# Performance work log

Measured on AMD Instinct MI355X. Metric: run time of the kernel, lower is better.

## Reference

```python
import jax, jax.numpy as jnp
import numpy as np

N_U, N_P, E, E_LAB = 100000, 50000, 2000000, 500000
D_U, D_P, H = 64, 128, 64


def _seg_mean(feat, idx, n):
    # scatter-mean: sum per destination / clamp(count, 1)
    s = jax.ops.segment_sum(feat, idx, num_segments=n)
    c = jax.ops.segment_sum(jnp.ones((idx.shape[0],), feat.dtype), idx, num_segments=n)
    return s / jnp.maximum(c, 1.0)[:, None]


def setup_inputs() -> dict:
    key = jax.random.key(0)
    ks = jax.random.split(key, 16)
    inp = {
        'x_user': jax.random.normal(ks[0], (N_U, D_U), jnp.float32),
        'x_product': jax.random.normal(ks[1], (N_P, D_P), jnp.float32),
        'W1_buys_l': jax.random.normal(ks[2], (D_U, H), jnp.float32) * 0.05,
        'b1_buys': jnp.zeros((H,), jnp.float32),
        'W1_buys_r': jax.random.normal(ks[3], (D_P, H), jnp.float32) * 0.05,
        'W1_rev_l': jax.random.normal(ks[4], (D_P, H), jnp.float32) * 0.05,
        'b1_rev': jnp.zeros((H,), jnp.float32),
        'W1_rev_r': jax.random.normal(ks[5], (D_U, H), jnp.float32) * 0.05,
        'W2_buys_l': jax.random.normal(ks[6], (H, H), jnp.float32) * 0.05,
        'b2_buys': jnp.zeros((H,), jnp.float32),
        'W2_buys_r': jax.random.normal(ks[7], (H, H), jnp.float32) * 0.05,
        'W2_rev_l': jax.random.normal(ks[8], (H, H), jnp.float32) * 0.05,
        'b2_rev': jnp.zeros((H,), jnp.float32),
        'W2_rev_r': jax.random.normal(ks[9], (H, H), jnp.float32) * 0.05,
        'edge_src': jax.random.randint(ks[10], (E,), 0, N_U, jnp.int32),
        'edge_dst': jax.random.randint(ks[11], (E,), 0, N_P, jnp.int32),
        'lab_u': jax.random.randint(ks[12], (E_LAB,), 0, N_U, jnp.int32),
        'lab_p': jax.random.randint(ks[13], (E_LAB,), 0, N_P, jnp.int32),
    }
    return inp


def reference(x_user, x_product, W1_buys_l, b1_buys, W1_buys_r, W1_rev_l, b1_rev, W1_rev_r,
              W2_buys_l, b2_buys, W2_buys_r, W2_rev_l, b2_rev, W2_rev_r,
              edge_src, edge_dst, lab_u, lab_p):
    # SAGEConv (mean aggr): out_dst = mean_agg(x_src) @ W_l + b + x_dst @ W_r
    def sage(x_src, x_dst, src, dst, n_dst, Wl, b, Wr):
        agg = _seg_mean(x_src[src], dst, n_dst)
        return agg @ Wl + b + x_dst @ Wr

    n_u, n_p = x_user.shape[0], x_product.shape[0]
    # layer 1 (per edge type, hetero) + relu
    h_p = jax.nn.relu(sage(x_user, x_product, edge_src, edge_dst, n_p, W1_buys_l, b1_buys, W1_buys_r))
    h_u = jax.nn.relu(sage(x_product, x_user, edge_dst, edge_src, n_u, W1_rev_l, b1_rev, W1_rev_r))
    # layer 2
    h_p2 = sage(h_u, h_p, edge_src, edge_dst, n_p, W2_buys_l, b2_buys, W2_buys_r)
    h_u2 = sage(h_p, h_u, edge_dst, edge_src, n_u, W2_rev_l, b2_rev, W2_rev_r)
    # classifier: per-label-edge dot product
    return jnp.sum(h_u2[lab_u] * h_p2[lab_p], axis=-1)
```

## Files before the change

kernel.cpp:

```cpp
#include <hip/hip_runtime.h>


using u16 = unsigned short;
using u32 = unsigned int;

__device__ __forceinline__ u16 bf16r(float f) {
    u32 b = __float_as_uint(f);
    b += 0x7fffu + ((b >> 16) & 1u);
    return (u16)(b >> 16);
}
__device__ __forceinline__ float2 bfup(u32 u) {
    return make_float2(__uint_as_float(u << 16), __uint_as_float(u & 0xffff0000u));
}

#define BSH 8
#define MAXB 512
#define CHUNK 4096
#define RPT 16

#define FMA_ROW(ACC, O, W4) \
    ACC[0] += (O) * (W4).x; ACC[1] += (O) * (W4).y; \
    ACC[2] += (O) * (W4).z; ACC[3] += (O) * (W4).w;

__global__ __launch_bounds__(256) void k_partCast(
    const int* __restrict__ keysP, const int* __restrict__ payP,
    int* __restrict__ curPp, uint2* __restrict__ pairsP, int NBP, int SLP,
    const int* __restrict__ keysU, const int* __restrict__ payU,
    int* __restrict__ curUp, uint2* __restrict__ pairsU, int NBU, int SLU,
    int E, int pblocks,
    const int* __restrict__ keysL,
    int* __restrict__ curLp, uint2* __restrict__ pairsL, int NBL, int SLL,
    int EL, int lblocks,
    const float* __restrict__ xc, u16* __restrict__ yc, int n8,
    int ctStart, int g128,
    const float* __restrict__ xp, const float* __restrict__ Wrl,
    const float* __restrict__ Wbr, u16* __restrict__ bfB,
    float* __restrict__ h_p, float* __restrict__ sinkF,
    u16* __restrict__ sinkB, int NPc) {
    __shared__ __align__(16) char smem[49664];
    int tid = threadIdx.x;
    int bix = blockIdx.x;
    if (bix >= ctStart) {
        float* Ws = (float*)smem;
        float* op = (float*)(smem + 32768);
        int cbix = bix - ctStart;
        const float* W; float* h; u16* hbf;
        int bid;
        if (cbix < g128) { W = Wrl; h = sinkF; hbf = bfB;   bid = cbix; }
        else             { W = Wbr; h = h_p;   hbf = sinkB; bid = cbix - g128; }
        for (int i = tid; i < 128 * 16; i += 256)
            ((float4*)Ws)[i] = ((const float4*)W)[i];
        const int c4 = (tid & 15) * 4;
        const int rb = (tid >> 4) * 2;
        const int ntiles = (NPc + 31) / 32;
        for (int tile = bid; tile < ntiles; tile += g128) {
            const int row0 = tile * 32;
            __syncthreads();
            for (int i = tid; i < 32 * 32; i += 256) {
                int r = i >> 5, k4 = (i & 31) * 4;
                int row = row0 + r;
                float4 v = make_float4(0.f, 0.f, 0.f, 0.f);
                if (row < NPc) v = *(const float4*)(xp + (size_t)row * 128 + k4);
                *(float4*)(op + r * 132 + k4) = v;
            }
            __syncthreads();
            float acc[2][4];
#pragma unroll
            for (int i = 0; i < 2; ++i) {
                acc[i][0] = 0.f; acc[i][1] = 0.f; acc[i][2] = 0.f; acc[i][3] = 0.f;
            }
            for (int kk = 0; kk < 128; kk += 4) {
                float4 w0 = *(const float4*)(Ws + (kk + 0) * 64 + c4);
                float4 w1 = *(const float4*)(Ws + (kk + 1) * 64 + c4);
                float4 w2 = *(const float4*)(Ws + (kk + 2) * 64 + c4);
                float4 w3 = *(const float4*)(Ws + (kk + 3) * 64 + c4);
#pragma unroll
                for (int i = 0; i < 2; ++i) {
                    float4 o = *(const float4*)(op + (rb + i) * 132 + kk);
                    FMA_ROW(acc[i], o.x, w0);
                    FMA_ROW(acc[i], o.y, w1);
                    FMA_ROW(acc[i], o.z, w2);
                    FMA_ROW(acc[i], o.w, w3);
                }
            }
#pragma unroll
            for (int i = 0; i < 2; ++i) {
                int row = row0 + rb + i;
                if (row >= NPc) continue;
                float v0 = acc[i][0], v1 = acc[i][1], v2 = acc[i][2], v3 = acc[i][3];
                *(float4*)(h + (size_t)row * 64 + c4) = make_float4(v0, v1, v2, v3);
                uint2 o;
                o.x = (u32)bf16r(v0) | ((u32)bf16r(v1) << 16);
                o.y = (u32)bf16r(v2) | ((u32)bf16r(v3) << 16);
                *(uint2*)(hbf + (size_t)row * 64 + c4) = o;
            }
        }
        return;
    }
    if (bix >= 2 * pblocks + lblocks) {
        int i = (bix - 2 * pblocks - lblocks) * 256 + tid;
        if (i < n8) {
            const float4* x4 = (const float4*)xc;
            float4 a = x4[i * 2], b = x4[i * 2 + 1];
            uint4 o;
            o.x = (u32)bf16r(a.x) | ((u32)bf16r(a.y) << 16);
            o.y = (u32)bf16r(a.z) | ((u32)bf16r(a.w) << 16);
            o.z = (u32)bf16r(b.x) | ((u32)bf16r(b.y) << 16);
            o.w = (u32)bf16r(b.z) | ((u32)bf16r(b.w) << 16);
            ((uint4*)yc)[i] = o;
        }
        return;
    }
    int* hist   = (int*)smem;
    int* sA     = (int*)(smem + 2048);
    int* sB     = (int*)(smem + 4096);
    int* bx     = (int*)(smem + 6144);
    int* gbase  = (int*)(smem + 8192);
    uint2* prs  = (uint2*)(smem + 10240);
    const int* keys; const int* pay; int* cursor; uint2* pairs;
    int NB, SL, cb, nE;
    if (bix < pblocks) {
        keys = keysP; pay = payP; cursor = curPp; pairs = pairsP; NB = NBP; SL = SLP;
        cb = bix; nE = E;
    } else if (bix < 2 * pblocks) {
        keys = keysU; pay = payU; cursor = curUp; pairs = pairsU; NB = NBU; SL = SLU;
        cb = bix - pblocks; nE = E;
    } else {
        keys = keysL; pay = nullptr; cursor = curLp; pairs = pairsL; NB = NBL; SL = SLL;
        cb = bix - 2 * pblocks; nE = EL;
    }
    int i0 = cb * CHUNK;
    int count = min(CHUNK, nE - i0);
    for (int i = tid; i < MAXB; i += 256) hist[i] = 0;
    __syncthreads();
    int keyr[RPT], payr[RPT], rankr[RPT];
#pragma unroll
    for (int r = 0; r < RPT; ++r) {
        int idx = r * 256 + tid;
        if (idx < count) {
            int k = keys[i0 + idx];
            keyr[r] = k;
            payr[r] = pay ? pay[i0 + idx] : (i0 + idx);
            rankr[r] = atomicAdd(&hist[k >> BSH], 1);
        } else keyr[r] = -1;
    }
    __syncthreads();
    sA[tid] = hist[tid]; sA[tid + 256] = hist[tid + 256];
    __syncthreads();
    int* src = sA; int* dst = sB;
    for (int off = 1; off < MAXB; off <<= 1) {
        dst[tid] = src[tid] + ((tid >= off) ? src[tid - off] : 0);
        int i2 = tid + 256;
        dst[i2] = src[i2] + ((i2 >= off) ? src[i2 - off] : 0);
        __syncthreads();
        int* t = src; src = dst; dst = t;
    }
    bx[tid] = src[tid] - hist[tid];
    bx[tid + 256] = src[tid + 256] - hist[tid + 256];
    __syncthreads();
    for (int b = tid; b < NB; b += 256) {
        int c = hist[b];
        gbase[b] = c ? (b * SL + atomicAdd(&cursor[b], c)) : 0;
    }
#pragma unroll
    for (int r = 0; r < RPT; ++r) {
        if (keyr[r] >= 0)
            prs[bx[keyr[r] >> BSH] + rankr[r]] = make_uint2((u32)keyr[r], (u32)payr[r]);
    }
    __syncthreads();
    for (int j = tid; j < count; j += 256) {
        uint2 pr = prs[j];
        int b = pr.x >> BSH;
        pairs[gbase[b] + (j - bx[b])] = pr;
    }
}

__global__ __launch_bounds__(256) void k_bucketFill(
    const uint2* __restrict__ pairsP, const int* __restrict__ cntP, int NBP, int SLP,
    int* __restrict__ nbr_p, int* __restrict__ deg_p, int* __restrict__ ptr_p, int NP,
    const uint2* __restrict__ pairsU, const int* __restrict__ cntU, int NBU, int SLU,
    int* __restrict__ nbr_u, int* __restrict__ deg_u, int* __restrict__ ptr_u, int NU) {
    const uint2* pairs; const int* cntA; int* nbr; int* deg; int* ptr;
    int N, SL, bucket;
    if ((int)blockIdx.x < NBP) {
        pairs = pairsP; cntA = cntP; nbr = nbr_p; deg = deg_p; ptr = ptr_p; N = NP;
        SL = SLP; bucket = blockIdx.x;
    } else {
        pairs = pairsU; cntA = cntU; nbr = nbr_u; deg = deg_u; ptr = ptr_u; N = NU;
        SL = SLU; bucket = blockIdx.x - NBP;
    }
    int tid = threadIdx.x;
    int base = bucket * SL;
    int cnt = cntA[bucket];
    __shared__ int h[256];
    __shared__ int s[256];
    __shared__ int cur[256];
    h[tid] = 0;
    __syncthreads();
    for (int j = tid; j < cnt; j += 256) atomicAdd(&h[pairs[base + j].x & 255], 1);
    __syncthreads();
    int d = h[tid];
    s[tid] = d;
    __syncthreads();
    for (int off = 1; off < 256; off <<= 1) {
        int v = (tid >= off) ? s[tid - off] : 0;
        __syncthreads();
        s[tid] += v;
        __syncthreads();
    }
    int excl = s[tid] - d;
    int node = bucket * 256 + tid;
    if (node < N) { deg[node] = d; ptr[node] = base + excl; }
    cur[tid] = excl;
    __syncthreads();
    for (int j = tid; j < cnt; j += 256) {
        uint2 pr = pairs[base + j];
        int pos = atomicAdd(&cur[pr.x & 255], 1);
        nbr[base + pos] = (int)(pr.y << 7);
    }
}

#define ACC8(A01,A23,A45,A67,V) \
    A01 += bfup((V).x); A23 += bfup((V).y); A45 += bfup((V).z); A67 += bfup((V).w);

__global__ __launch_bounds__(256) void k_gather2(
    const u16* __restrict__ yA, const int* __restrict__ nbrA, const int* __restrict__ stpA,
    const int* __restrict__ degA, float* __restrict__ aggA, int NA,
    const u16* __restrict__ yB, const int* __restrict__ nbrB, const int* __restrict__ stpB,
    const int* __restrict__ degB, float* __restrict__ aggB, int NB) {
    int w = (blockIdx.x * 256 + threadIdx.x) >> 6;
    int lane = threadIdx.x & 63;
    if (w >= NA + NB) return;
    const u16* y; const int* nbr; const int* stp; const int* deg; float* agg; int n;
    if (w < NA) { y = yA; nbr = nbrA; stp = stpA; deg = degA; agg = aggA; n = w; }
    else        { y = yB; nbr = nbrB; stp = stpB; deg = degB; agg = aggB; n = w - NA; }
    const int q = lane >> 3, t = lane & 7;
    const int d = deg[n];
    const int st = stp[n];
    const char* yb = (const char*)y + t * 16;
    float2 a01 = make_float2(0.f, 0.f), a23 = make_float2(0.f, 0.f);
    float2 a45 = make_float2(0.f, 0.f), a67 = make_float2(0.f, 0.f);
    for (int j = 0; j < d; j += 64) {
        const int cnt = min(d - j, 64);
        int offv = 0;
        if (lane < cnt) offv = nbr[st + j + lane];
#define GLD(R) \
        int g##R = __shfl(offv, R * 8 + q, 64); \
        uint4 v##R = make_uint4(0u, 0u, 0u, 0u); \
        if (R * 8 + q < cnt) v##R = *(const uint4*)(yb + g##R);
        GLD(0) GLD(1) GLD(2) GLD(3) GLD(4) GLD(5) GLD(6) GLD(7)
#undef GLD
#define ACCR(R) if (R * 8 < cnt) { ACC8(a01,a23,a45,a67,v##R) }
        ACCR(0) ACCR(1) ACCR(2) ACCR(3) ACCR(4) ACCR(5) ACCR(6) ACCR(7)
#undef ACCR
    }
#pragma unroll
    for (int m = 8; m < 64; m <<= 1) {
        a01.x += __shfl_xor(a01.x, m, 64); a01.y += __shfl_xor(a01.y, m, 64);
        a23.x += __shfl_xor(a23.x, m, 64); a23.y += __shfl_xor(a23.y, m, 64);
        a45.x += __shfl_xor(a45.x, m, 64); a45.y += __shfl_xor(a45.y, m, 64);
        a67.x += __shfl_xor(a67.x, m, 64); a67.y += __shfl_xor(a67.y, m, 64);
    }
    if (q == 0) {
        float dinv = 1.0f / (float)max(d, 1);
        float* dstp = agg + n * 64 + t * 8;
        *(float4*)dstp       = make_float4(a01.x * dinv, a01.y * dinv, a23.x * dinv, a23.y * dinv);
        *(float4*)(dstp + 4) = make_float4(a45.x * dinv, a45.y * dinv, a67.x * dinv, a67.y * dinv);
    }
}

template <int K, bool PRE, bool BIAS, bool RELU, bool EMIT>
__global__ __launch_bounds__(256) void k_ctilePairX(
    const float* __restrict__ pre0, const float* __restrict__ bias0,
    const float* __restrict__ x0, const float* __restrict__ W0,
    float* __restrict__ h0, u16* __restrict__ hbf0, int N0, int g0,
    const float* __restrict__ pre1, const float* __restrict__ bias1,
    const float* __restrict__ x1, const float* __restrict__ W1,
    float* __restrict__ h1, u16* __restrict__ hbf1, int N1) {
    constexpr int ROWS = (K == 64) ? 64 : 32;
    constexpr int RR = ROWS / 16;
    constexpr int STRIDE = K + 4;
    constexpr int KF4 = K / 4;
    __shared__ float Ws[K * 64];
    __shared__ float op[ROWS * STRIDE];
    const float* pre; const float* bias; const float* x; const float* W;
    float* h; u16* hbf;
    int N, bid, gsz;
    if ((int)blockIdx.x < g0) {
        pre = pre0; bias = bias0; x = x0; W = W0; h = h0; hbf = hbf0; N = N0;
        bid = blockIdx.x; gsz = g0;
    } else {
        pre = pre1; bias = bias1; x = x1; W = W1; h = h1; hbf = hbf1; N = N1;
        bid = blockIdx.x - g0; gsz = gridDim.x - g0;
    }
    const int tid = threadIdx.x;
    for (int i = tid; i < K * 16; i += 256)
        ((float4*)Ws)[i] = ((const float4*)W)[i];
    const int c4 = (tid & 15) * 4;
    const int rb = (tid >> 4) * RR;
    float bx_ = 0.f, by_ = 0.f, bz_ = 0.f, bw_ = 0.f;
    if (BIAS) {
        float4 b4 = *(const float4*)(bias + c4);
        bx_ = b4.x; by_ = b4.y; bz_ = b4.z; bw_ = b4.w;
    }
    const int ntiles = (N + ROWS - 1) / ROWS;
    for (int tile = bid; tile < ntiles; tile += gsz) {
        const int row0 = tile * ROWS;
        __syncthreads();
        for (int i = tid; i < ROWS * KF4; i += 256) {
            int r = i / KF4, k4 = (i % KF4) * 4;
            int row = row0 + r;
            float4 v = make_float4(0.f, 0.f, 0.f, 0.f);
            if (row < N) v = *(const float4*)(x + (size_t)row * K + k4);
            *(float4*)(op + r * STRIDE + k4) = v;
        }
        __syncthreads();
        float acc[RR][4];
#pragma unroll
        for (int i = 0; i < RR; ++i) {
            float px = 0.f, py = 0.f, pz = 0.f, pw = 0.f;
            if (PRE) {
                int row = row0 + rb + i;
                if (row < N) {
                    float4 p = *(const float4*)(pre + row * 64 + c4);
                    px = p.x; py = p.y; pz = p.z; pw = p.w;
                }
            }
            acc[i][0] = bx_ + px; acc[i][1] = by_ + py;
            acc[i][2] = bz_ + pz; acc[i][3] = bw_ + pw;
        }
        for (int kk = 0; kk < K; kk += 4) {
            float4 w0 = *(const float4*)(Ws + (kk + 0) * 64 + c4);
            float4 w1 = *(const float4*)(Ws + (kk + 1) * 64 + c4);
            float4 w2 = *(const float4*)(Ws + (kk + 2) * 64 + c4);
            float4 w3 = *(const float4*)(Ws + (kk + 3) * 64 + c4);
#pragma unroll
            for (int i = 0; i < RR; ++i) {
                float4 o = *(const float4*)(op + (rb + i) * STRIDE + kk);
                FMA_ROW(acc[i], o.x, w0);
                FMA_ROW(acc[i], o.y, w1);
                FMA_ROW(acc[i], o.z, w2);
                FMA_ROW(acc[i], o.w, w3);
            }
        }
#pragma unroll
        for (int i = 0; i < RR; ++i) {
            int row = row0 + rb + i;
            if (row >= N) continue;
            float v0 = acc[i][0], v1 = acc[i][1], v2 = acc[i][2], v3 = acc[i][3];
            if (RELU) {
                v0 = fmaxf(v0, 0.f); v1 = fmaxf(v1, 0.f);
                v2 = fmaxf(v2, 0.f); v3 = fmaxf(v3, 0.f);
            }
            *(float4*)(h + row * 64 + c4) = make_float4(v0, v1, v2, v3);
            if (EMIT) {
                uint2 o;
                o.x = (u32)bf16r(v0) | ((u32)bf16r(v1) << 16);
                o.y = (u32)bf16r(v2) | ((u32)bf16r(v3) << 16);
                *(uint2*)(hbf + row * 64 + c4) = o;
            }
        }
    }
}

template <bool BIAS>
__global__ __launch_bounds__(256) void k_ctilePairCat(
    const float* __restrict__ bias0, const float* __restrict__ xa0,
    const float* __restrict__ xb0, const float* __restrict__ Wa0,
    const float* __restrict__ Wb0, float* __restrict__ h0, int N0, int g0,
    const float* __restrict__ bias1, const float* __restrict__ xa1,
    const float* __restrict__ xb1, const float* __restrict__ Wa1,
    const float* __restrict__ Wb1, float* __restrict__ h1, int N1) {
    constexpr int ROWS = 32, RR = 2, STRIDE = 132, KF4 = 32;
    __shared__ float Ws[128 * 64];
    __shared__ float op[ROWS * STRIDE];
    const float* bias; const float* xa; const float* xb;
    const float* Wa; const float* Wb; float* h;
    int N, bid, gsz;
    if ((int)blockIdx.x < g0) {
        bias = bias0; xa = xa0; xb = xb0; Wa = Wa0; Wb = Wb0; h = h0; N = N0;
        bid = blockIdx.x; gsz = g0;
    } else {
        bias = bias1; xa = xa1; xb = xb1; Wa = Wa1; Wb = Wb1; h = h1; N = N1;
        bid = blockIdx.x - g0; gsz = gridDim.x - g0;
    }
    const int tid = threadIdx.x;
    for (int i = tid; i < 64 * 16; i += 256) {
        ((float4*)Ws)[i]           = ((const float4*)Wa)[i];
        ((float4*)Ws)[64 * 16 + i] = ((const float4*)Wb)[i];
    }
    const int c4 = (tid & 15) * 4;
    const int rb = (tid >> 4) * RR;
    float bx_ = 0.f, by_ = 0.f, bz_ = 0.f, bw_ = 0.f;
    if (BIAS) {
        float4 b4 = *(const float4*)(bias + c4);
        bx_ = b4.x; by_ = b4.y; bz_ = b4.z; bw_ = b4.w;
    }
    const int ntiles = (N + ROWS - 1) / ROWS;
    for (int tile = bid; tile < ntiles; tile += gsz) {
        const int row0 = tile * ROWS;
        __syncthreads();
        for (int i = tid; i < ROWS * KF4; i += 256) {
            int r = i >> 5, k4 = (i & 31) * 4;
            int row = row0 + r;
            float4 v = make_float4(0.f, 0.f, 0.f, 0.f);
            if (row < N)
                v = (k4 < 64) ? *(const float4*)(xa + (size_t)row * 64 + k4)
                              : *(const float4*)(xb + (size_t)row * 64 + (k4 - 64));
            *(float4*)(op + r * STRIDE + k4) = v;
        }
        __syncthreads();
        float acc[RR][4];
#pragma unroll
        for (int i = 0; i < RR; ++i) {
            acc[i][0] = bx_; acc[i][1] = by_; acc[i][2] = bz_; acc[i][3] = bw_;
        }
        for (int kk = 0; kk < 128; kk += 4) {
            float4 w0 = *(const float4*)(Ws + (kk + 0) * 64 + c4);
            float4 w1 = *(const float4*)(Ws + (kk + 1) * 64 + c4);
            float4 w2 = *(const float4*)(Ws + (kk + 2) * 64 + c4);
            float4 w3 = *(const float4*)(Ws + (kk + 3) * 64 + c4);
#pragma unroll
            for (int i = 0; i < RR; ++i) {
                float4 o = *(const float4*)(op + (rb + i) * STRIDE + kk);
                FMA_ROW(acc[i], o.x, w0);
                FMA_ROW(acc[i], o.y, w1);
                FMA_ROW(acc[i], o.z, w2);
                FMA_ROW(acc[i], o.w, w3);
            }
        }
#pragma unroll
        for (int i = 0; i < RR; ++i) {
            int row = row0 + rb + i;
            if (row >= N) continue;
            *(float4*)(h + row * 64 + c4) =
                make_float4(acc[i][0], acc[i][1], acc[i][2], acc[i][3]);
        }
    }
}

__global__ __launch_bounds__(256) void k_classifyS(const float* __restrict__ hu,
                                                   const float* __restrict__ hp,
                                                   const int* __restrict__ lu,
                                                   const uint2* __restrict__ pairsL,
                                                   const int* __restrict__ cntL,
                                                   int lsh,
                                                   float* __restrict__ out, int nslots) {
    int w = (blockIdx.x * 256 + threadIdx.x) >> 6;
    int lane = threadIdx.x & 63;
    int q = lane >> 4, t = lane & 15;
    int slot = w * 4 + q;
    float v = 0.f;
    int e = 0;
    bool ok = false;
    if (slot < nslots) {
        int bucket = slot >> lsh;
        int within = slot & ((1 << lsh) - 1);
        if (within < cntL[bucket]) {
            uint2 pr = pairsL[slot];
            int p = (int)pr.x;
            e = (int)pr.y;
            int u = lu[e];
            float4 a = *(const float4*)(hu + (size_t)u * 64 + t * 4);
            float4 b = *(const float4*)(hp + (size_t)p * 64 + t * 4);
            v = a.x * b.x + a.y * b.y + a.z * b.z + a.w * b.w;
            ok = true;
        }
    }
#pragma unroll
    for (int m = 1; m < 16; m <<= 1) v += __shfl_xor(v, m, 64);
    if (t == 0 && ok) out[e] = v;
}

extern "C" void kernel_launch(void* const* d_in, const int* in_sizes, int n_in,
                              void* d_out, int out_size, void* d_ws, size_t ws_size,
                              hipStream_t stream) {
    const float* x_user    = (const float*)d_in[0];
    const float* x_product = (const float*)d_in[1];
    const float* W1bl = (const float*)d_in[2];
    const float* b1b  = (const float*)d_in[3];
    const float* W1br = (const float*)d_in[4];
    const float* W1rl = (const float*)d_in[5];
    const float* b1r  = (const float*)d_in[6];
    const float* W1rr = (const float*)d_in[7];
    const float* W2bl = (const float*)d_in[8];
    const float* b2b  = (const float*)d_in[9];
    const float* W2br = (const float*)d_in[10];
    const float* W2rl = (const float*)d_in[11];
    const float* b2r  = (const float*)d_in[12];
    const float* W2rr = (const float*)d_in[13];
    const int* esrc = (const int*)d_in[14];
    const int* edst = (const int*)d_in[15];
    const int* lu   = (const int*)d_in[16];
    const int* lp   = (const int*)d_in[17];

    const int NU = in_sizes[0] / 64;
    const int NP = in_sizes[1] / 128;
    const int E  = in_sizes[14];
    const int EL = in_sizes[16];
    const int NBP = (NP + 255) >> BSH;
    const int NBU = (NU + 255) >> BSH;
    const int NBL = NBP;

    const int SLP = E / NBP + E / (NBP * 8) + 1024;
    const int SLU = E / NBU + E / (NBU * 8) + 1024;
    int lneed = EL / NBL + EL / (NBL * 4) + 512;
    int lsh = 1;
    while ((1 << lsh) < lneed) ++lsh;
    const int SLL = 1 << lsh;

    char* ws = (char*)d_ws;
    size_t off = 0;
    auto alloc = [&](size_t bytes) -> void* {
        void* p = ws + off;
        off += (bytes + 255) & ~(size_t)255;
        return p;
    };
    int*   deg_u  = (int*)alloc((size_t)NU * 4);
    int*   deg_p  = (int*)alloc((size_t)NP * 4);
    int*   ptr_u  = (int*)alloc((size_t)NU * 4);
    int*   ptr_p  = (int*)alloc((size_t)NP * 4);
    int*   curP   = (int*)alloc((size_t)MAXB * 4);
    int*   curU   = (int*)alloc((size_t)MAXB * 4);
    int*   curL   = (int*)alloc((size_t)MAXB * 4);
    int*   nbr_u  = (int*)alloc((size_t)NBU * SLU * 4);
    int*   nbr_p  = (int*)alloc((size_t)NBP * SLP * 4);
    uint2* pairsL = (uint2*)alloc((size_t)NBL * SLL * 8);
    size_t aggBytes = (size_t)(NP + NU) * 64 * 4;
    size_t pairBytes = ((size_t)NBP * SLP + (size_t)NBU * SLU) * 8;
    char* uni = (char*)alloc(aggBytes > pairBytes ? aggBytes : pairBytes);
    float* aggP   = (float*)uni;
    float* aggU   = (float*)(uni + (size_t)NP * 64 * 4);
    uint2* pairsP = (uint2*)uni;
    uint2* pairsU = (uint2*)(uni + (size_t)NBP * SLP * 8);
    u16*   bfA    = (u16*)alloc((size_t)NU * 64 * 2);
    u16*   bfB    = (u16*)alloc((size_t)NP * 64 * 2);
    float* h_p    = (float*)alloc((size_t)NP * 64 * 4);
    float* h_u    = (float*)alloc((size_t)NU * 64 * 4);
    float* sinkF  = h_u;
    u16*   sinkB  = (u16*)((char*)h_u + (size_t)NP * 64 * 4);

    const int tP32 = (NP + 31) / 32;
    const int tU32 = (NU + 31) / 32;
    const int tP64 = (NP + 63) / 64, tU64 = (NU + 63) / 64;
    auto cap = [](int t, int c) { return t < c ? t : c; };

    hipMemsetAsync(curP, 0, (size_t)MAXB * 3 * 4, stream);
    const int n8 = NU * 64 / 8;
    const int castBlocks = (n8 + 255) / 256;
    const int pblocks = (E + CHUNK - 1) / CHUNK;
    const int lblocks = (EL + CHUNK - 1) / CHUNK;
    const int g128 = cap(tP32, 768);
    const int ctStart = 2 * pblocks + lblocks + castBlocks;
    k_partCast<<<ctStart + 2 * g128, 256, 0, stream>>>(
        edst, esrc, curP, pairsP, NBP, SLP,
        esrc, edst, curU, pairsU, NBU, SLU, E, pblocks,
        lp, curL, pairsL, NBL, SLL, EL, lblocks,
        x_user, bfA, n8,
        ctStart, g128,
        x_product, W1rl, W1br, bfB, h_p, sinkF, sinkB, NP);
    k_bucketFill<<<NBP + NBU, 256, 0, stream>>>(
        pairsP, curP, NBP, SLP, nbr_p, deg_p, ptr_p, NP,
        pairsU, curU, NBU, SLU, nbr_u, deg_u, ptr_u, NU);

    k_gather2<<<(NP + NU + 3) / 4, 256, 0, stream>>>(bfA, nbr_p, ptr_p, deg_p, aggP, NP,
                                                     bfB, nbr_u, ptr_u, deg_u, aggU, NU);
    {
        const int gP = cap(tP64, 512), gU = cap(tU64, 1024);
        k_ctilePairX<64, true, true, true, true><<<gP + gU, 256, 0, stream>>>(
            h_p, b1b, aggP, W1bl, h_p, bfB, NP, gP,
            aggU, b1r, x_user, W1rr, h_u, bfA, NU);
    }

    k_gather2<<<(NP + NU + 3) / 4, 256, 0, stream>>>(bfA, nbr_p, ptr_p, deg_p, aggP, NP,
                                                     bfB, nbr_u, ptr_u, deg_u, aggU, NU);
    {
        const int gP = cap(tP32, 512), gU = cap(tU32, 1024);
        k_ctilePairCat<true><<<gP + gU, 256, 0, stream>>>(
            b2b, aggP, h_p, W2bl, W2br, h_p, NP, gP,
            b2r, aggU, h_u, W2rl, W2rr, h_u, NU);
    }

    const int nslots = NBL << lsh;
    k_classifyS<<<((nslots + 3) / 4 + 3) / 4, 256, 0, stream>>>(
        h_u, h_p, lu, pairsL, curL, lsh, (float*)d_out, nslots);
}
```

Measured before the change: 481.2 us.

## Replace bucket-sort CSR build with direct atomic scatter into fixed-slot adjacency

Drops the two-pass partition plus bucket-fill CSR construction. Each edge is now scattered straight into a fixed-capacity per-node slot array using a global atomicAdd on a per-node counter, and the gather reads from node*SL with degree min(cnt, SL). The label-edge sort is also removed, so the classifier reads lu/lp directly. This cuts one kernel launch and the sort traffic, but relies on node degrees staying under 2*avg+48 or 2*avg+24. Edges past that capacity are silently dropped while the count still includes them, so the mean is wrong for high-degree nodes.

```diff
diff --git a/kernel.cpp b/kernel.cpp
--- a/kernel.cpp
+++ b/kernel.cpp
@@ -13,41 +13,29 @@
     return make_float2(__uint_as_float(u << 16), __uint_as_float(u & 0xffff0000u));
 }
 
-#define BSH 8
-#define MAXB 512
-#define CHUNK 4096
-#define RPT 16
-
 #define FMA_ROW(ACC, O, W4) \
     ACC[0] += (O) * (W4).x; ACC[1] += (O) * (W4).y; \
     ACC[2] += (O) * (W4).z; ACC[3] += (O) * (W4).w;
 
-__global__ __launch_bounds__(256) void k_partCast(
-    const int* __restrict__ keysP, const int* __restrict__ payP,
-    int* __restrict__ curPp, uint2* __restrict__ pairsP, int NBP, int SLP,
-    const int* __restrict__ keysU, const int* __restrict__ payU,
-    int* __restrict__ curUp, uint2* __restrict__ pairsU, int NBU, int SLU,
-    int E, int pblocks,
-    const int* __restrict__ keysL,
-    int* __restrict__ curLp, uint2* __restrict__ pairsL, int NBL, int SLL,
-    int EL, int lblocks,
-    const float* __restrict__ xc, u16* __restrict__ yc, int n8,
-    int ctStart, int g128,
+__global__ __launch_bounds__(256) void k_buildAll(
+    const int* __restrict__ esrc, const int* __restrict__ edst, int E,
+    int* __restrict__ cntP, int* __restrict__ nbrP, int SLPn,
+    int* __restrict__ cntU, int* __restrict__ nbrU, int SLUn,
+    int g128, int sStart, int cStart, int NPc,
     const float* __restrict__ xp, const float* __restrict__ Wrl,
     const float* __restrict__ Wbr, u16* __restrict__ bfB,
-    float* __restrict__ h_p, float* __restrict__ sinkF,
-    u16* __restrict__ sinkB, int NPc) {
+    float* __restrict__ h_p, float* __restrict__ sinkF, u16* __restrict__ sinkB,
+    const float* __restrict__ xc, u16* __restrict__ yc, int n8) {
     __shared__ __align__(16) char smem[49664];
     int tid = threadIdx.x;
     int bix = blockIdx.x;
-    if (bix >= ctStart) {
+    if (bix < 2 * g128) {
         float* Ws = (float*)smem;
         float* op = (float*)(smem + 32768);
-        int cbix = bix - ctStart;
         const float* W; float* h; u16* hbf;
         int bid;
-        if (cbix < g128) { W = Wrl; h = sinkF; hbf = bfB;   bid = cbix; }
-        else             { W = Wbr; h = h_p;   hbf = sinkB; bid = cbix - g128; }
+        if (bix < g128) { W = Wrl; h = sinkF; hbf = bfB;   bid = bix; }
+        else            { W = Wbr; h = h_p;   hbf = sinkB; bid = bix - g128; }
         for (int i = tid; i < 128 * 16; i += 256)
             ((float4*)Ws)[i] = ((const float4*)W)[i];
         const int c4 = (tid & 15) * 4;
@@ -97,126 +85,36 @@
         }
         return;
     }
-    if (bix >= 2 * pblocks + lblocks) {
-        int i = (bix - 2 * pblocks - lblocks) * 256 + tid;
-        if (i < n8) {
-            const float4* x4 = (const float4*)xc;
-            float4 a = x4[i * 2], b = x4[i * 2 + 1];
-            uint4 o;
-            o.x = (u32)bf16r(a.x) | ((u32)bf16r(a.y) << 16);
-            o.y = (u32)bf16r(a.z) | ((u32)bf16r(a.w) << 16);
-            o.z = (u32)bf16r(b.x) | ((u32)bf16r(b.y) << 16);
-            o.w = (u32)bf16r(b.z) | ((u32)bf16r(b.w) << 16);
-            ((uint4*)yc)[i] = o;
-        }
+    if (bix < cStart) {
+        int i = (bix - sStart) * 256 + tid;
+        int E4 = E >> 2;
+#define SCAT(U, P) { \
+        int pp = atomicAdd(&cntP[P], 1); \
+        if (pp < SLPn) nbrP[(size_t)(P) * SLPn + pp] = (U) << 7; \
+        int pu = atomicAdd(&cntU[U], 1); \
+        if (pu < SLUn) nbrU[(size_t)(U) * SLUn + pu] = (P) << 7; }
+        if (i < E4) {
+            int4 s = ((const int4*)esrc)[i];
+            int4 d = ((const int4*)edst)[i];
+            SCAT(s.x, d.x) SCAT(s.y, d.y) SCAT(s.z, d.z) SCAT(s.w, d.w)
+        }
+        if (bix == sStart && tid < (E & 3)) {
+            int e = E4 * 4 + tid;
+            SCAT(esrc[e], edst[e])
+        }
+#undef SCAT
         return;
     }
-    int* hist   = (int*)smem;
-    int* sA     = (int*)(smem + 2048);
-    int* sB     = (int*)(smem + 4096);
-    int* bx     = (int*)(smem + 6144);
-    int* gbase  = (int*)(smem + 8192);
-    uint2* prs  = (uint2*)(smem + 10240);
-    const int* keys; const int* pay; int* cursor; uint2* pairs;
-    int NB, SL, cb, nE;
-    if (bix < pblocks) {
-        keys = keysP; pay = payP; cursor = curPp; pairs = pairsP; NB = NBP; SL = SLP;
-        cb = bix; nE = E;
-    } else if (bix < 2 * pblocks) {
-        keys = keysU; pay = payU; cursor = curUp; pairs = pairsU; NB = NBU; SL = SLU;
-        cb = bix - pblocks; nE = E;
-    } else {
-        keys = keysL; pay = nullptr; cursor = curLp; pairs = pairsL; NB = NBL; SL = SLL;
-        cb = bix - 2 * pblocks; nE = EL;
-    }
-    int i0 = cb * CHUNK;
-    int count = min(CHUNK, nE - i0);
-    for (int i = tid; i < MAXB; i += 256) hist[i] = 0;
-    __syncthreads();
-    int keyr[RPT], payr[RPT], rankr[RPT];
-#pragma unroll
-    for (int r = 0; r < RPT; ++r) {
-        int idx = r * 256 + tid;
-        if (idx < count) {
-            int k = keys[i0 + idx];
-            keyr[r] = k;
-            payr[r] = pay ? pay[i0 + idx] : (i0 + idx);
-            rankr[r] = atomicAdd(&hist[k >> BSH], 1);
-        } else keyr[r] = -1;
-    }
-    __syncthreads();
-    sA[tid] = hist[tid]; sA[tid + 256] = hist[tid + 256];
-    __syncthreads();
-    int* src = sA; int* dst = sB;
-    for (int off = 1; off < MAXB; off <<= 1) {
-        dst[tid] = src[tid] + ((tid >= off) ? src[tid - off] : 0);
-        int i2 = tid + 256;
-        dst[i2] = src[i2] + ((i2 >= off) ? src[i2 - off] : 0);
-        __syncthreads();
-        int* t = src; src = dst; dst = t;
-    }
-    bx[tid] = src[tid] - hist[tid];
-    bx[tid + 256] = src[tid + 256] - hist[tid + 256];
-    __syncthreads();
-    for (int b = tid; b < NB; b += 256) {
-        int c = hist[b];
-        gbase[b] = c ? (b * SL + atomicAdd(&cursor[b], c)) : 0;
-    }
-#pragma unroll
-    for (int r = 0; r < RPT; ++r) {
-        if (keyr[r] >= 0)
-            prs[bx[keyr[r] >> BSH] + rankr[r]] = make_uint2((u32)keyr[r], (u32)payr[r]);
-    }
-    __syncthreads();
-    for (int j = tid; j < count; j += 256) {
-        uint2 pr = prs[j];
-        int b = pr.x >> BSH;
-        pairs[gbase[b] + (j - bx[b])] = pr;
-    }
-}
-
-__global__ __launch_bounds__(256) void k_bucketFill(
-    const uint2* __restrict__ pairsP, const int* __restrict__ cntP, int NBP, int SLP,
-    int* __restrict__ nbr_p, int* __restrict__ deg_p, int* __restrict__ ptr_p, int NP,
-    const uint2* __restrict__ pairsU, const int* __restrict__ cntU, int NBU, int SLU,
-    int* __restrict__ nbr_u, int* __restrict__ deg_u, int* __restrict__ ptr_u, int NU) {
-    const uint2* pairs; const int* cntA; int* nbr; int* deg; int* ptr;
-    int N, SL, bucket;
-    if ((int)blockIdx.x < NBP) {
-        pairs = pairsP; cntA = cntP; nbr = nbr_p; deg = deg_p; ptr = ptr_p; N = NP;
-        SL = SLP; bucket = blockIdx.x;
-    } else {
-        pairs = pairsU; cntA = cntU; nbr = nbr_u; deg = deg_u; ptr = ptr_u; N = NU;
-        SL = SLU; bucket = blockIdx.x - NBP;
-    }
-    int tid = threadIdx.x;
-    int base = bucket * SL;
-    int cnt = cntA[bucket];
-    __shared__ int h[256];
-    __shared__ int s[256];
-    __shared__ int cur[256];
-    h[tid] = 0;
-    __syncthreads();
-    for (int j = tid; j < cnt; j += 256) atomicAdd(&h[pairs[base + j].x & 255], 1);
-    __syncthreads();
-    int d = h[tid];
-    s[tid] = d;
-    __syncthreads();
-    for (int off = 1; off < 256; off <<= 1) {
-        int v = (tid >= off) ? s[tid - off] : 0;
-        __syncthreads();
-        s[tid] += v;
-        __syncthreads();
-    }
-    int excl = s[tid] - d;
-    int node = bucket * 256 + tid;
-    if (node < N) { deg[node] = d; ptr[node] = base + excl; }
-    cur[tid] = excl;
-    __syncthreads();
-    for (int j = tid; j < cnt; j += 256) {
-        uint2 pr = pairs[base + j];
-        int pos = atomicAdd(&cur[pr.x & 255], 1);
-        nbr[base + pos] = (int)(pr.y << 7);
+    int i = (bix - cStart) * 256 + tid;
+    if (i < n8) {
+        const float4* x4 = (const float4*)xc;
+        float4 a = x4[i * 2], b = x4[i * 2 + 1];
+        uint4 o;
+        o.x = (u32)bf16r(a.x) | ((u32)bf16r(a.y) << 16);
+        o.y = (u32)bf16r(a.z) | ((u32)bf16r(a.w) << 16);
+        o.z = (u32)bf16r(b.x) | ((u32)bf16r(b.y) << 16);
+        o.w = (u32)bf16r(b.z) | ((u32)bf16r(b.w) << 16);
+        ((uint4*)yc)[i] = o;
     }
 }
 
@@ -224,19 +122,19 @@
     A01 += bfup((V).x); A23 += bfup((V).y); A45 += bfup((V).z); A67 += bfup((V).w);
 
 __global__ __launch_bounds__(256) void k_gather2(
-    const u16* __restrict__ yA, const int* __restrict__ nbrA, const int* __restrict__ stpA,
-    const int* __restrict__ degA, float* __restrict__ aggA, int NA,
-    const u16* __restrict__ yB, const int* __restrict__ nbrB, const int* __restrict__ stpB,
-    const int* __restrict__ degB, float* __restrict__ aggB, int NB) {
+    const u16* __restrict__ yA, const int* __restrict__ nbrA,
+    const int* __restrict__ cntA, int SLA, float* __restrict__ aggA, int NA,
+    const u16* __restrict__ yB, const int* __restrict__ nbrB,
+    const int* __restrict__ cntB, int SLB, float* __restrict__ aggB, int NB) {
     int w = (blockIdx.x * 256 + threadIdx.x) >> 6;
     int lane = threadIdx.x & 63;
     if (w >= NA + NB) return;
-    const u16* y; const int* nbr; const int* stp; const int* deg; float* agg; int n;
-    if (w < NA) { y = yA; nbr = nbrA; stp = stpA; deg = degA; agg = aggA; n = w; }
-    else        { y = yB; nbr = nbrB; stp = stpB; deg = degB; agg = aggB; n = w - NA; }
+    const u16* y; const int* nbr; const int* cntp; float* agg; int n, SL;
+    if (w < NA) { y = yA; nbr = nbrA; cntp = cntA; agg = aggA; n = w; SL = SLA; }
+    else        { y = yB; nbr = nbrB; cntp = cntB; agg = aggB; n = w - NA; SL = SLB; }
     const int q = lane >> 3, t = lane & 7;
-    const int d = deg[n];
-    const int st = stp[n];
+    const int d = min(cntp[n], SL);
+    const int st = n * SL;
     const char* yb = (const char*)y + t * 16;
     float2 a01 = make_float2(0.f, 0.f), a23 = make_float2(0.f, 0.f);
     float2 a45 = make_float2(0.f, 0.f), a67 = make_float2(0.f, 0.f);
@@ -439,37 +337,25 @@
     }
 }
 
-__global__ __launch_bounds__(256) void k_classifyS(const float* __restrict__ hu,
+__global__ __launch_bounds__(256) void k_classify4(const float* __restrict__ hu,
                                                    const float* __restrict__ hp,
                                                    const int* __restrict__ lu,
-                                                   const uint2* __restrict__ pairsL,
-                                                   const int* __restrict__ cntL,
-                                                   int lsh,
-                                                   float* __restrict__ out, int nslots) {
+                                                   const int* __restrict__ lp,
+                                                   float* __restrict__ out, int EL) {
     int w = (blockIdx.x * 256 + threadIdx.x) >> 6;
     int lane = threadIdx.x & 63;
     int q = lane >> 4, t = lane & 15;
-    int slot = w * 4 + q;
+    int e = w * 4 + q;
     float v = 0.f;
-    int e = 0;
-    bool ok = false;
-    if (slot < nslots) {
-        int bucket = slot >> lsh;
-        int within = slot & ((1 << lsh) - 1);
-        if (within < cntL[bucket]) {
-            uint2 pr = pairsL[slot];
-            int p = (int)pr.x;
-            e = (int)pr.y;
-            int u = lu[e];
-            float4 a = *(const float4*)(hu + (size_t)u * 64 + t * 4);
-            float4 b = *(const float4*)(hp + (size_t)p * 64 + t * 4);
-            v = a.x * b.x + a.y * b.y + a.z * b.z + a.w * b.w;
-            ok = true;
-        }
+    if (e < EL) {
+        int u = lu[e], p = lp[e];
+        float4 a = *(const float4*)(hu + (size_t)u * 64 + t * 4);
+        float4 b = *(const float4*)(hp + (size_t)p * 64 + t * 4);
+        v = a.x * b.x + a.y * b.y + a.z * b.z + a.w * b.w;
     }
 #pragma unroll
     for (int m = 1; m < 16; m <<= 1) v += __shfl_xor(v, m, 64);
-    if (t == 0 && ok) out[e] = v;
+    if (t == 0 && e < EL) out[e] = v;
 }
 
 extern "C" void kernel_launch(void* const* d_in, const int* in_sizes, int n_in,
@@ -498,16 +384,9 @@
     const int NP = in_sizes[1] / 128;
     const int E  = in_sizes[14];
     const int EL = in_sizes[16];
-    const int NBP = (NP + 255) >> BSH;
-    const int NBU = (NU + 255) >> BSH;
-    const int NBL = NBP;
-
-    const int SLP = E / NBP + E / (NBP * 8) + 1024;
-    const int SLU = E / NBU + E / (NBU * 8) + 1024;
-    int lneed = EL / NBL + EL / (NBL * 4) + 512;
-    int lsh = 1;
-    while ((1 << lsh) < lneed) ++lsh;
-    const int SLL = 1 << lsh;
+
+    const int SLPn = 2 * (E / NP) + 48;
+    const int SLUn = 2 * (E / NU) + 24;
 
     char* ws = (char*)d_ws;
     size_t off = 0;
@@ -516,23 +395,12 @@
         off += (bytes + 255) & ~(size_t)255;
         return p;
     };
-    int*   deg_u  = (int*)alloc((size_t)NU * 4);
-    int*   deg_p  = (int*)alloc((size_t)NP * 4);
-    int*   ptr_u  = (int*)alloc((size_t)NU * 4);
-    int*   ptr_p  = (int*)alloc((size_t)NP * 4);
-    int*   curP   = (int*)alloc((size_t)MAXB * 4);
-    int*   curU   = (int*)alloc((size_t)MAXB * 4);
-    int*   curL   = (int*)alloc((size_t)MAXB * 4);
-    int*   nbr_u  = (int*)alloc((size_t)NBU * SLU * 4);
-    int*   nbr_p  = (int*)alloc((size_t)NBP * SLP * 4);
-    uint2* pairsL = (uint2*)alloc((size_t)NBL * SLL * 8);
-    size_t aggBytes = (size_t)(NP + NU) * 64 * 4;
-    size_t pairBytes = ((size_t)NBP * SLP + (size_t)NBU * SLU) * 8;
-    char* uni = (char*)alloc(aggBytes > pairBytes ? aggBytes : pairBytes);
-    float* aggP   = (float*)uni;
-    float* aggU   = (float*)(uni + (size_t)NP * 64 * 4);
-    uint2* pairsP = (uint2*)uni;
-    uint2* pairsU = (uint2*)(uni + (size_t)NBP * SLP * 8);
+    int*   cntP   = (int*)alloc(((size_t)NP + NU) * 4);
+    int*   cntU   = cntP + NP;
+    int*   nbr_p  = (int*)alloc((size_t)NP * SLPn * 4);
+    int*   nbr_u  = (int*)alloc((size_t)NU * SLUn * 4);
+    float* aggP   = (float*)alloc((size_t)NP * 64 * 4);
+    float* aggU   = (float*)alloc((size_t)NU * 64 * 4);
     u16*   bfA    = (u16*)alloc((size_t)NU * 64 * 2);
     u16*   bfB    = (u16*)alloc((size_t)NP * 64 * 2);
     float* h_p    = (float*)alloc((size_t)NP * 64 * 4);
@@ -545,26 +413,24 @@
     const int tP64 = (NP + 63) / 64, tU64 = (NU + 63) / 64;
     auto cap = [](int t, int c) { return t < c ? t : c; };
 
-    hipMemsetAsync(curP, 0, (size_t)MAXB * 3 * 4, stream);
+    hipMemsetAsync(cntP, 0, ((size_t)NP + NU) * 4, stream);
     const int n8 = NU * 64 / 8;
     const int castBlocks = (n8 + 255) / 256;
-    const int pblocks = (E + CHUNK - 1) / CHUNK;
-    const int lblocks = (EL + CHUNK - 1) / CHUNK;
+    const int sblocks = ((E >> 2) + 255) / 256;
     const int g128 = cap(tP32, 768);
-    const int ctStart = 2 * pblocks + lblocks + castBlocks;
-    k_partCast<<<ctStart + 2 * g128, 256, 0, stream>>>(
-        edst, esrc, curP, pairsP, NBP, SLP,
-        esrc, edst, curU, pairsU, NBU, SLU, E, pblocks,
-        lp, curL, pairsL, NBL, SLL, EL, lblocks,
-        x_user, bfA, n8,
-        ctStart, g128,
-        x_product, W1rl, W1br, bfB, h_p, sinkF, sinkB, NP);
-    k_bucketFill<<<NBP + NBU, 256, 0, stream>>>(
-        pairsP, curP, NBP, SLP, nbr_p, deg_p, ptr_p, NP,
-        pairsU, curU, NBU, SLU, nbr_u, deg_u, ptr_u, NU);
-
-    k_gather2<<<(NP + NU + 3) / 4, 256, 0, stream>>>(bfA, nbr_p, ptr_p, deg_p, aggP, NP,
-                                                     bfB, nbr_u, ptr_u, deg_u, aggU, NU);
+    const int sStart = 2 * g128;
+    const int cStart = sStart + sblocks;
+    k_buildAll<<<cStart + castBlocks, 256, 0, stream>>>(
+        esrc, edst, E,
+        cntP, nbr_p, SLPn,
+        cntU, nbr_u, SLUn,
+        g128, sStart, cStart, NP,
+        x_product, W1rl, W1br, bfB, h_p, sinkF, sinkB,
+        x_user, bfA, n8);
+
+    k_gather2<<<(NP + NU + 3) / 4, 256, 0, stream>>>(
+        bfA, nbr_p, cntP, SLPn, aggP, NP,
+        bfB, nbr_u, cntU, SLUn, aggU, NU);
     {
         const int gP = cap(tP64, 512), gU = cap(tU64, 1024);
         k_ctilePairX<64, true, true, true, true><<<gP + gU, 256, 0, stream>>>(
@@ -572,8 +438,9 @@
             aggU, b1r, x_user, W1rr, h_u, bfA, NU);
     }
 
-    k_gather2<<<(NP + NU + 3) / 4, 256, 0, stream>>>(bfA, nbr_p, ptr_p, deg_p, aggP, NP,
-                                                     bfB, nbr_u, ptr_u, deg_u, aggU, NU);
+    k_gather2<<<(NP + NU + 3) / 4, 256, 0, stream>>>(
+        bfA, nbr_p, cntP, SLPn, aggP, NP,
+        bfB, nbr_u, cntU, SLUn, aggU, NU);
     {
         const int gP = cap(tP32, 512), gU = cap(tU32, 1024);
         k_ctilePairCat<true><<<gP + gU, 256, 0, stream>>>(
@@ -581,7 +448,6 @@
             b2r, aggU, h_u, W2rl, W2rr, h_u, NU);
     }
 
-    const int nslots = NBL << lsh;
-    k_classifyS<<<((nslots + 3) / 4 + 3) / 4, 256, 0, stream>>>(
-        h_u, h_p, lu, pairsL, curL, lsh, (float*)d_out, nslots);
-}
+    k_classify4<<<((EL + 3) / 4 + 3) / 4, 256, 0, stream>>>(
+        h_u, h_p, lu, lp, (float*)d_out, EL);
+}
```

Measured after the change: 751.4 us. 1.56x slower.

## Pack bucket pairs into 32-bit words and halve partition shared memory

Applied to the files above, without the earlier changes.

Each (key, payload) pair used in the bucket partition is packed into one 32-bit word: the low 8 key bits go in the top byte and the payload in the low 24 bits. This halves the global pair buffer traffic in partition, bucket fill and classify. Because the bucket id is no longer stored, scatter recovers it by binary search over the bucket offsets. The GEMM path now stages the weight matrix in two 64-row halves, shrinking shared memory from about 49KB to 33KB to allow more resident blocks, at the cost of extra syncs and a reload of the weights per tile.

```diff
diff --git a/kernel.cpp b/kernel.cpp
--- a/kernel.cpp
+++ b/kernel.cpp
@@ -24,12 +24,12 @@
 
 __global__ __launch_bounds__(256) void k_partCast(
     const int* __restrict__ keysP, const int* __restrict__ payP,
-    int* __restrict__ curPp, uint2* __restrict__ pairsP, int NBP, int SLP,
+    int* __restrict__ curPp, u32* __restrict__ pairsP, int NBP, int SLP,
     const int* __restrict__ keysU, const int* __restrict__ payU,
-    int* __restrict__ curUp, uint2* __restrict__ pairsU, int NBU, int SLU,
+    int* __restrict__ curUp, u32* __restrict__ pairsU, int NBU, int SLU,
     int E, int pblocks,
     const int* __restrict__ keysL,
-    int* __restrict__ curLp, uint2* __restrict__ pairsL, int NBL, int SLL,
+    int* __restrict__ curLp, u32* __restrict__ pairsL, int NBL, int SLL,
     int EL, int lblocks,
     const float* __restrict__ xc, u16* __restrict__ yc, int n8,
     int ctStart, int g128,
@@ -37,19 +37,17 @@
     const float* __restrict__ Wbr, u16* __restrict__ bfB,
     float* __restrict__ h_p, float* __restrict__ sinkF,
     u16* __restrict__ sinkB, int NPc) {
-    __shared__ __align__(16) char smem[49664];
+    __shared__ __align__(16) char smem[33280];
     int tid = threadIdx.x;
     int bix = blockIdx.x;
     if (bix >= ctStart) {
         float* Ws = (float*)smem;
-        float* op = (float*)(smem + 32768);
+        float* op = (float*)(smem + 16384);
         int cbix = bix - ctStart;
         const float* W; float* h; u16* hbf;
         int bid;
         if (cbix < g128) { W = Wrl; h = sinkF; hbf = bfB;   bid = cbix; }
         else             { W = Wbr; h = h_p;   hbf = sinkB; bid = cbix - g128; }
-        for (int i = tid; i < 128 * 16; i += 256)
-            ((float4*)Ws)[i] = ((const float4*)W)[i];
         const int c4 = (tid & 15) * 4;
         const int rb = (tid >> 4) * 2;
         const int ntiles = (NPc + 31) / 32;
@@ -63,24 +61,30 @@
                 if (row < NPc) v = *(const float4*)(xp + (size_t)row * 128 + k4);
                 *(float4*)(op + r * 132 + k4) = v;
             }
-            __syncthreads();
             float acc[2][4];
 #pragma unroll
             for (int i = 0; i < 2; ++i) {
                 acc[i][0] = 0.f; acc[i][1] = 0.f; acc[i][2] = 0.f; acc[i][3] = 0.f;
             }
-            for (int kk = 0; kk < 128; kk += 4) {
-                float4 w0 = *(const float4*)(Ws + (kk + 0) * 64 + c4);
-                float4 w1 = *(const float4*)(Ws + (kk + 1) * 64 + c4);
-                float4 w2 = *(const float4*)(Ws + (kk + 2) * 64 + c4);
-                float4 w3 = *(const float4*)(Ws + (kk + 3) * 64 + c4);
-#pragma unroll
-                for (int i = 0; i < 2; ++i) {
-                    float4 o = *(const float4*)(op + (rb + i) * 132 + kk);
-                    FMA_ROW(acc[i], o.x, w0);
-                    FMA_ROW(acc[i], o.y, w1);
-                    FMA_ROW(acc[i], o.z, w2);
-                    FMA_ROW(acc[i], o.w, w3);
+            for (int half = 0; half < 2; ++half) {
+                __syncthreads();
+                for (int i = tid; i < 64 * 16; i += 256)
+                    ((float4*)Ws)[i] = ((const float4*)(W + half * 64 * 64))[i];
+                __syncthreads();
+                const int kb = half * 64;
+                for (int kk = 0; kk < 64; kk += 4) {
+                    float4 w0 = *(const float4*)(Ws + (kk + 0) * 64 + c4);
+                    float4 w1 = *(const float4*)(Ws + (kk + 1) * 64 + c4);
+                    float4 w2 = *(const float4*)(Ws + (kk + 2) * 64 + c4);
+                    float4 w3 = *(const float4*)(Ws + (kk + 3) * 64 + c4);
+#pragma unroll
+                    for (int i = 0; i < 2; ++i) {
+                        float4 o = *(const float4*)(op + (rb + i) * 132 + kb + kk);
+                        FMA_ROW(acc[i], o.x, w0);
+                        FMA_ROW(acc[i], o.y, w1);
+                        FMA_ROW(acc[i], o.z, w2);
+                        FMA_ROW(acc[i], o.w, w3);
+                    }
                 }
             }
 #pragma unroll
@@ -116,8 +120,8 @@
     int* sB     = (int*)(smem + 4096);
     int* bx     = (int*)(smem + 6144);
     int* gbase  = (int*)(smem + 8192);
-    uint2* prs  = (uint2*)(smem + 10240);
-    const int* keys; const int* pay; int* cursor; uint2* pairs;
+    u32* prs    = (u32*)(smem + 10240);
+    const int* keys; const int* pay; int* cursor; u32* pairs;
     int NB, SL, cb, nE;
     if (bix < pblocks) {
         keys = keysP; pay = payP; cursor = curPp; pairs = pairsP; NB = NBP; SL = SLP;
@@ -165,22 +169,26 @@
 #pragma unroll
     for (int r = 0; r < RPT; ++r) {
         if (keyr[r] >= 0)
-            prs[bx[keyr[r] >> BSH] + rankr[r]] = make_uint2((u32)keyr[r], (u32)payr[r]);
+            prs[bx[keyr[r] >> BSH] + rankr[r]] =
+                ((u32)(keyr[r] & 255) << 24) | (u32)payr[r];
     }
     __syncthreads();
     for (int j = tid; j < count; j += 256) {
-        uint2 pr = prs[j];
-        int b = pr.x >> BSH;
-        pairs[gbase[b] + (j - bx[b])] = pr;
+        int lo = 0, hi = NB - 1;
+        while (lo < hi) {
+            int mid = (lo + hi + 1) >> 1;
+            if (bx[mid] <= j) lo = mid; else hi = mid - 1;
+        }
+        pairs[gbase[lo] + (j - bx[lo])] = prs[j];
     }
 }
 
 __global__ __launch_bounds__(256) void k_bucketFill(
-    const uint2* __restrict__ pairsP, const int* __restrict__ cntP, int NBP, int SLP,
+    const u32* __restrict__ pairsP, const int* __restrict__ cntP, int NBP, int SLP,
     int* __restrict__ nbr_p, int* __restrict__ deg_p, int* __restrict__ ptr_p, int NP,
-    const uint2* __restrict__ pairsU, const int* __restrict__ cntU, int NBU, int SLU,
+    const u32* __restrict__ pairsU, const int* __restrict__ cntU, int NBU, int SLU,
     int* __restrict__ nbr_u, int* __restrict__ deg_u, int* __restrict__ ptr_u, int NU) {
-    const uint2* pairs; const int* cntA; int* nbr; int* deg; int* ptr;
+    const u32* pairs; const int* cntA; int* nbr; int* deg; int* ptr;
     int N, SL, bucket;
     if ((int)blockIdx.x < NBP) {
         pairs = pairsP; cntA = cntP; nbr = nbr_p; deg = deg_p; ptr = ptr_p; N = NP;
@@ -197,7 +205,7 @@
     __shared__ int cur[256];
     h[tid] = 0;
     __syncthreads();
-    for (int j = tid; j < cnt; j += 256) atomicAdd(&h[pairs[base + j].x & 255], 1);
+    for (int j = tid; j < cnt; j += 256) atomicAdd(&h[pairs[base + j] >> 24], 1);
     __syncthreads();
     int d = h[tid];
     s[tid] = d;
@@ -214,9 +222,9 @@
     cur[tid] = excl;
     __syncthreads();
     for (int j = tid; j < cnt; j += 256) {
-        uint2 pr = pairs[base + j];
-        int pos = atomicAdd(&cur[pr.x & 255], 1);
-        nbr[base + pos] = (int)(pr.y << 7);
+        u32 pr = pairs[base + j];
+        int pos = atomicAdd(&cur[pr >> 24], 1);
+        nbr[base + pos] = (int)((pr & 0xFFFFFFu) << 7);
     }
 }
 
@@ -442,7 +450,7 @@
 __global__ __launch_bounds__(256) void k_classifyS(const float* __restrict__ hu,
                                                    const float* __restrict__ hp,
                                                    const int* __restrict__ lu,
-                                                   const uint2* __restrict__ pairsL,
+                                                   const u32* __restrict__ pairsL,
                                                    const int* __restrict__ cntL,
                                                    int lsh,
                                                    float* __restrict__ out, int nslots) {
@@ -457,9 +465,9 @@
         int bucket = slot >> lsh;
         int within = slot & ((1 << lsh) - 1);
         if (within < cntL[bucket]) {
-            uint2 pr = pairsL[slot];
-            int p = (int)pr.x;
-            e = (int)pr.y;
+            u32 pr = pairsL[slot];
+            int p = (bucket << 8) | (int)(pr >> 24);
+            e = (int)(pr & 0xFFFFFFu);
             int u = lu[e];
             float4 a = *(const float4*)(hu + (size_t)u * 64 + t * 4);
             float4 b = *(const float4*)(hp + (size_t)p * 64 + t * 4);
@@ -520,19 +528,19 @@
     int*   deg_p  = (int*)alloc((size_t)NP * 4);
     int*   ptr_u  = (int*)alloc((size_t)NU * 4);
     int*   ptr_p  = (int*)alloc((size_t)NP * 4);
-    int*   curP   = (int*)alloc((size_t)MAXB * 4);
-    int*   curU   = (int*)alloc((size_t)MAXB * 4);
-    int*   curL   = (int*)alloc((size_t)MAXB * 4);
+    int*   curP   = (int*)alloc((size_t)MAXB * 3 * 4);
+    int*   curU   = curP + MAXB;
+    int*   curL   = curP + 2 * MAXB;
     int*   nbr_u  = (int*)alloc((size_t)NBU * SLU * 4);
     int*   nbr_p  = (int*)alloc((size_t)NBP * SLP * 4);
-    uint2* pairsL = (uint2*)alloc((size_t)NBL * SLL * 8);
+    u32*   pairsL = (u32*)alloc((size_t)NBL * SLL * 4);
     size_t aggBytes = (size_t)(NP + NU) * 64 * 4;
-    size_t pairBytes = ((size_t)NBP * SLP + (size_t)NBU * SLU) * 8;
+    size_t pairBytes = ((size_t)NBP * SLP + (size_t)NBU * SLU) * 4;
     char* uni = (char*)alloc(aggBytes > pairBytes ? aggBytes : pairBytes);
     float* aggP   = (float*)uni;
     float* aggU   = (float*)(uni + (size_t)NP * 64 * 4);
-    uint2* pairsP = (uint2*)uni;
-    uint2* pairsU = (uint2*)(uni + (size_t)NBP * SLP * 8);
+    u32*   pairsP = (u32*)uni;
+    u32*   pairsU = (u32*)(uni + (size_t)NBP * SLP * 4);
     u16*   bfA    = (u16*)alloc((size_t)NU * 64 * 2);
     u16*   bfB    = (u16*)alloc((size_t)NP * 64 * 2);
     float* h_p    = (float*)alloc((size_t)NP * 64 * 4);
```

Measured after the change: 1.076 ms. 124% more time.
